# Kernel tuning notes

Measured on AMD Instinct MI355X. Metric: run time of the kernel, lower is better.

## Reference

```python
import jax, jax.numpy as jnp
import numpy as np

B, T, C, H = 4, 2048, 1024, 16
HD = C // H


def setup_inputs() -> dict:
    key = jax.random.key(0)
    ks = jax.random.split(key, 9)
    s = 1.0 / np.sqrt(C)
    return {
        "x": jax.random.normal(ks[0], (B, T, C), dtype=jnp.float32),
        "Wk": jax.random.uniform(ks[1], (C, C), jnp.float32, -s, s),
        "bk": jax.random.uniform(ks[2], (C,), jnp.float32, -s, s),
        "Wq": jax.random.uniform(ks[3], (C, C), jnp.float32, -s, s),
        "bq": jax.random.uniform(ks[4], (C,), jnp.float32, -s, s),
        "Wv": jax.random.uniform(ks[5], (C, C), jnp.float32, -s, s),
        "bv": jax.random.uniform(ks[6], (C,), jnp.float32, -s, s),
        "Wp": jax.random.uniform(ks[7], (C, C), jnp.float32, -s, s),
        "bp": jax.random.uniform(ks[8], (C,), jnp.float32, -s, s),
        "padding_mask": jnp.ones((B, T), dtype=jnp.int32),
    }


def reference(x, Wk, bk, Wq, bq, Wv, bv, Wp, bp, padding_mask):
    # torch nn.Linear: y = x @ W.T + b  (W is [out, in])
    def split_heads(t):  # [B,T,C] -> [B,H,T,HD]
        return t.reshape(B, T, H, HD).transpose(0, 2, 1, 3)

    k = split_heads(x @ Wk.T + bk)
    q = split_heads(x @ Wq.T + bq)
    v = split_heads(x @ Wv.T + bv)

    scale = 1.0 / jnp.sqrt(jnp.float32(HD))
    att = jnp.einsum("bhqd,bhkd->bhqk", q, k) * scale  # [B,H,T,T]

    causal = jnp.tril(jnp.ones((T, T), dtype=bool))  # [T,T]
    pad = (padding_mask != 0)[:, None, None, :]       # [B,1,1,T]
    mask = causal[None, None, :, :] & pad
    att = jnp.where(mask, att, -jnp.inf)
    att = jax.nn.softmax(att, axis=-1)

    y = jnp.einsum("bhqk,bhkd->bhqd", att, v)  # [B,H,T,HD]
    y = y.transpose(0, 2, 1, 3).reshape(B, T, C)
    return y @ Wp.T + bp
```

## Files before the change

kernel.cpp:

```cpp
#include <hip/hip_runtime.h>
#include <hip/hip_bf16.h>
#include <math.h>
#include <stdint.h>

#define BB 4
#define TT 2048
#define CC 1024
#define HH 16
#define HD 64
#define MM (BB*TT)
#define NQT2 16
#define SCQ 0.180336878f

using f32x2  = __attribute__((ext_vector_type(2))) float;
using f32x4  = __attribute__((ext_vector_type(4))) float;
using f32x16 = __attribute__((ext_vector_type(16))) float;
using i32x4  = __attribute__((ext_vector_type(4))) int;
using bf16x4 = __attribute__((ext_vector_type(4))) __bf16;
using bf16x8 = __attribute__((ext_vector_type(8))) __bf16;

__device__ __forceinline__ float fast_exp2(float x) {
  return __builtin_amdgcn_exp2f(x);
}

__device__ __forceinline__ int cvt_pk_bf16(float lo, float hi_) {
  int r;
  asm("v_cvt_pk_bf16_f32 %0, %1, %2" : "=v"(r) : "v"(lo), "v"(hi_));
  return r;
}

__device__ __forceinline__ f32x2 max2(f32x2 a, f32x2 b) {
  return __builtin_elementwise_max(a, b);
}

__device__ __forceinline__ void gload_lds16(const void* g, void* l) {
  __builtin_amdgcn_global_load_lds(
      (__attribute__((address_space(1))) void*)(void*)(g),
      (__attribute__((address_space(3))) void*)(l), 16, 0, 0);
}

__global__ __launch_bounds__(256)
void cvt_f32_bf16(const float* __restrict__ s, __bf16* __restrict__ d, int n4) {
  int i = blockIdx.x * 256 + threadIdx.x;
  if (i >= n4) return;
  float4 v = ((const float4*)s)[i];
  bf16x4 o;
  o[0] = (__bf16)v.x; o[1] = (__bf16)v.y; o[2] = (__bf16)v.z; o[3] = (__bf16)v.w;
  *(bf16x4*)(d + (size_t)i * 4) = o;
}

__global__ __launch_bounds__(256)
void cvt_w4(const float* __restrict__ Wq, const float* __restrict__ Wk,
            const float* __restrict__ Wv, const float* __restrict__ Wp,
            __bf16* __restrict__ wqkv, __bf16* __restrict__ wpb) {
  int which = blockIdx.y;
  const float* s = which == 0 ? Wq : which == 1 ? Wk : which == 2 ? Wv : Wp;
  __bf16* d = which == 3 ? wpb : wqkv + (size_t)which * CC * CC;
  float sc = which == 0 ? SCQ : 1.f;
  int i = blockIdx.x * 256 + threadIdx.x;
  float4 v = ((const float4*)s)[i];
  bf16x4 o;
  o[0] = (__bf16)(v.x * sc); o[1] = (__bf16)(v.y * sc);
  o[2] = (__bf16)(v.z * sc); o[3] = (__bf16)(v.w * sc);
  *(bf16x4*)(d + (size_t)i * 4) = o;
}

#define WAITV6 asm volatile("s_waitcnt vmcnt(6)" ::: "memory")
#define WAITV4 asm volatile("s_waitcnt vmcnt(4)" ::: "memory")
#define WAITV0 asm volatile("s_waitcnt vmcnt(0)" ::: "memory")
#define WAITL0 asm volatile("s_waitcnt lgkmcnt(0)" ::: "memory")
#define BARR   __builtin_amdgcn_s_barrier()
#define SB0    __builtin_amdgcn_sched_barrier(0)
#define PRIO1  __builtin_amdgcn_s_setprio(1)
#define PRIO0  __builtin_amdgcn_s_setprio(0)

#define LDA_SET(buf, mq)                                                      \
  {                                                                           \
    const char* base_ = (const char*)&LA[buf][mq][0] + (wm * 64 + lq) * 128;  \
    _Pragma("unroll")                                                         \
    for (int m4 = 0; m4 < 4; ++m4)                                            \
      _Pragma("unroll")                                                       \
      for (int kk = 0; kk < 2; ++kk)                                          \
        a[m4 * 2 + kk] =                                                      \
            *(const bf16x8*)(base_ + m4 * 2048 + ((kk * 64 + g * 16) ^ swz)); \
  }

#define LDB_SET(buf, nq)                                                      \
  {                                                                           \
    const char* base_ = (const char*)&LB[buf][nq][0] + (wn * 32 + lq) * 128;  \
    _Pragma("unroll")                                                         \
    for (int n2 = 0; n2 < 2; ++n2)                                            \
      _Pragma("unroll")                                                       \
      for (int kk = 0; kk < 2; ++kk)                                          \
        b[nq][n2 * 2 + kk] =                                                  \
            *(const bf16x8*)(base_ + n2 * 2048 + ((kk * 64 + g * 16) ^ swz)); \
  }

#define STAGE_A(nbuf, h, tt)                                                  \
  {                                                                           \
    const char* s_ = Ag + ((size_t)((h)*128 + srow)) * 2048 + (tt)*128 + scol1; \
    gload_lds16(s_, (char*)&LA[nbuf][h][0] + so16);                           \
    gload_lds16(s_ + (size_t)64 * 2048, (char*)&LA[nbuf][h][0] + so16 + 8192);\
  }

#define STAGE_B(nbuf, h, tt)                                                  \
  {                                                                           \
    const char* s_ = Bg + ((size_t)((h)*128 + srow)) * 2048 + (tt)*128 + scol1; \
    gload_lds16(s_, (char*)&LB[nbuf][h][0] + so16);                           \
    gload_lds16(s_ + (size_t)64 * 2048, (char*)&LB[nbuf][h][0] + so16 + 8192);\
  }

#define MFMA_PH(mq, nq)                                                       \
  _Pragma("unroll")                                                           \
  for (int m4 = 0; m4 < 4; ++m4)                                              \
    _Pragma("unroll")                                                         \
    for (int n2 = 0; n2 < 2; ++n2)                                            \
      _Pragma("unroll")                                                       \
      for (int kk = 0; kk < 2; ++kk)                                          \
        acc[mq][m4][nq][n2] = __builtin_amdgcn_mfma_f32_16x16x32_bf16(        \
            a[m4 * 2 + kk], b[nq][n2 * 2 + kk], acc[mq][m4][nq][n2], 0, 0, 0);

__global__ __launch_bounds__(512, 2)
void gemm_qkv(const __bf16* __restrict__ A, const __bf16* __restrict__ Bm,
              const float* __restrict__ b0, const float* __restrict__ b1,
              const float* __restrict__ b2, __bf16* __restrict__ out,
              __bf16* __restrict__ vt) {
  __shared__ __bf16 LA[2][2][128 * 64];
  __shared__ __bf16 LB[2][2][128 * 64];
  const int tid = threadIdx.x, wid = tid >> 6, lane = tid & 63;
  const int g = lane >> 4, lq = lane & 15;
  const int wm = wid >> 2, wn = wid & 3;
  const int bx0 = blockIdx.x;
  const int bx = (bx0 & 7) * 48 + (bx0 >> 3);
  const int bm = bx / 12, bn = bx % 12;
  const int brow = bm << 8, bcol = bn << 8;
  const int swz = (lq & 7) << 4;

  const int srow = tid >> 3, so16 = tid * 16;
  const int scol1 = ((tid & 7) << 4) ^ ((srow & 7) << 4);
  const char* Ag = (const char*)A + (size_t)brow * 2048;
  const char* Bg = (const char*)Bm + (size_t)bcol * 2048;

  f32x4 acc[2][4][2][2] = {};
  bf16x8 a[8], b[2][4];

  STAGE_A(0, 0, 0); STAGE_B(0, 0, 0); STAGE_B(0, 1, 0); STAGE_A(0, 1, 0);
  STAGE_A(1, 0, 1); STAGE_B(1, 0, 1); STAGE_B(1, 1, 1);
  WAITV6; BARR;

#pragma unroll 1
  for (int t = 0; t < 8; ++t) {
    const bool s2 = (t < 7);
    const int k1 = 2 * t + 1, k2 = 2 * t + 2, k3 = 2 * t + 3;
    LDA_SET(0, 0); LDB_SET(0, 0);
    STAGE_A(1, 1, k1);
    BARR; WAITL0; SB0;
    PRIO1; MFMA_PH(0, 0); PRIO0; BARR;
    LDB_SET(0, 1);
    if (s2) STAGE_A(0, 0, k2);
    BARR; WAITL0; SB0;
    PRIO1; MFMA_PH(0, 1); PRIO0; BARR;
    LDA_SET(0, 1);
    if (s2) STAGE_B(0, 0, k2);
    BARR; WAITL0; SB0;
    PRIO1; MFMA_PH(1, 1); PRIO0; BARR;
    if (s2) { STAGE_B(0, 1, k2); WAITV6; } else { WAITV0; }
    BARR; SB0;
    PRIO1; MFMA_PH(1, 0); PRIO0; BARR;
    LDA_SET(1, 0); LDB_SET(1, 0);
    if (s2) STAGE_A(0, 1, k2);
    BARR; WAITL0; SB0;
    PRIO1; MFMA_PH(0, 0); PRIO0; BARR;
    LDB_SET(1, 1);
    if (s2) STAGE_A(1, 0, k3);
    BARR; WAITL0; SB0;
    PRIO1; MFMA_PH(0, 1); PRIO0; BARR;
    LDA_SET(1, 1);
    if (s2) STAGE_B(1, 0, k3);
    BARR; WAITL0; SB0;
    PRIO1; MFMA_PH(1, 1); PRIO0; BARR;
    if (s2) { STAGE_B(1, 1, k3); WAITV6; }
    BARR; SB0;
    PRIO1; MFMA_PH(1, 0); PRIO0; BARR;
  }

  const int proj = bn >> 2;
  if (proj < 2) {
    const float* bias = proj == 0 ? b0 : b1;
    const float bsc = proj == 0 ? SCQ : 1.f;
#pragma unroll
    for (int mq = 0; mq < 2; ++mq)
#pragma unroll
      for (int nq = 0; nq < 2; ++nq)
#pragma unroll
        for (int n2 = 0; n2 < 2; ++n2) {
          int col = bcol + nq * 128 + wn * 32 + n2 * 16 + lq;
          int cw = col & (CC - 1);
          float bb = bias[cw] * bsc;
          int h_ = cw >> 6, d_ = cw & (HD - 1);
#pragma unroll
          for (int m4 = 0; m4 < 4; ++m4) {
            int row0 = brow + mq * 128 + wm * 64 + m4 * 16 + g * 4;
#pragma unroll
            for (int i = 0; i < 4; ++i) {
              int row = row0 + i;
              int b_ = row >> 11, t_ = row & (TT - 1);
              out[((size_t)proj << 23) +
                  ((((size_t)b_ * HH + h_) * TT + t_) << 6) + d_] =
                  (__bf16)(acc[mq][m4][nq][n2][i] + bb);
            }
          }
        }
  } else {
    __bf16* lt = (__bf16*)&LA[0][0][0];
    const int cv0 = (bn & 3) << 8;
    const int b_ = brow >> 11, t0 = brow & (TT - 1);
    const int hbase = (bn & 3) << 2;
    const int rd_d = tid >> 3, rd_tb = (tid & 7) << 5;
#pragma unroll
    for (int cc = 0; cc < 4; ++cc) {
      if ((wn >> 1) == (cc & 1)) {
#pragma unroll
        for (int n2 = 0; n2 < 2; ++n2) {
          int c = ((wn & 1) << 5) + (n2 << 4) + lq;
          float bb = b2[cv0 + (cc << 6) + c];
#pragma unroll
          for (int mq = 0; mq < 2; ++mq)
#pragma unroll
            for (int m4 = 0; m4 < 4; ++m4) {
              int r = (mq << 7) + (wm << 6) + (m4 << 4) + (g << 2);
              bf16x4 pk;
#pragma unroll
              for (int i = 0; i < 4; ++i)
                pk[i] = (__bf16)(acc[mq][m4][cc >> 1][n2][i] + bb);
              *(bf16x4*)(lt + c * 264 + r) = pk;
            }
        }
      }
      __syncthreads();
      __bf16* dst = vt + (((size_t)((b_ * HH + hbase + cc) * HD + rd_d)) << 11)
                       + t0 + rd_tb;
      const __bf16* srcl = lt + rd_d * 264 + rd_tb;
#pragma unroll
      for (int j = 0; j < 4; ++j)
        *(bf16x8*)(dst + j * 8) = *(const bf16x8*)(srcl + j * 8);
      __syncthreads();
    }
  }
}

__global__ __launch_bounds__(256, 2)
void gemm_proj(const __bf16* __restrict__ A, const __bf16* __restrict__ Bm,
               const float* __restrict__ bias, float* __restrict__ out,
               int M, int N, int K) {
  __shared__ __bf16 As[128 * 32];
  __shared__ __bf16 Bs[128 * 32];
  const int tid = threadIdx.x;
  const int wid = tid >> 6, lane = tid & 63;
  const int g = lane >> 4, lq = lane & 15;
  const int nbn = N >> 7;
  int bx = blockIdx.x;
  const int nb = gridDim.x;
  if ((nb & 7) == 0) { const int q = nb >> 3; bx = (bx & 7) * q + (bx >> 3); }
  const int brow = (bx / nbn) << 7;
  const int bcol = (bx % nbn) << 7;
  const int wr = (wid >> 1) << 6, wc = (wid & 1) << 6;

  f32x4 acc[4][4] = {};

  const int o0 = wid * 2048 + lane * 16;
  for (int kt = 0; kt < K; kt += 32) {
    __syncthreads();
#pragma unroll
    for (int j = 0; j < 2; ++j) {
      int o = o0 + j * 1024;
      int row = o >> 6, colb = o & 63;
      gload_lds16((const char*)A + ((size_t)(brow + row) * K + kt) * 2 + colb,
                  (char*)As + o);
      gload_lds16((const char*)Bm + ((size_t)(bcol + row) * K + kt) * 2 + colb,
                  (char*)Bs + o);
    }
    __syncthreads();
    bf16x8 av[4], bv[4];
#pragma unroll
    for (int m = 0; m < 4; ++m)
      av[m] = *(const bf16x8*)(As + (wr + m * 16 + lq) * 32 + g * 8);
#pragma unroll
    for (int n = 0; n < 4; ++n)
      bv[n] = *(const bf16x8*)(Bs + (wc + n * 16 + lq) * 32 + g * 8);
#pragma unroll
    for (int m = 0; m < 4; ++m)
#pragma unroll
      for (int n = 0; n < 4; ++n)
        acc[m][n] = __builtin_amdgcn_mfma_f32_16x16x32_bf16(av[m], bv[n], acc[m][n], 0, 0, 0);
  }

#pragma unroll
  for (int m = 0; m < 4; ++m) {
#pragma unroll
    for (int n = 0; n < 4; ++n) {
      int col = bcol + wc + n * 16 + lq;
      float bb = bias[col];
      int row0 = brow + wr + m * 16 + g * 4;
#pragma unroll
      for (int i = 0; i < 4; ++i)
        out[(size_t)(row0 + i) * N + col] = acc[m][n][i] + bb;
    }
  }
}

__global__ __launch_bounds__(256, 4)
void attn_fwd(const __bf16* __restrict__ Q, const __bf16* __restrict__ K,
              const __bf16* __restrict__ Vt, const int* __restrict__ pm,
              __bf16* __restrict__ Y) {
  __shared__ __bf16 Ks[2][64 * 64];
  __shared__ __bf16 Vs[2][64 * 64];
  __shared__ int flg;
  const int tid = threadIdx.x, wid = tid >> 6, lane = tid & 63;
  const int l31 = lane & 31, hi = lane >> 5;
  const int bx = blockIdx.x;
  const int bh = bx & 63, jj = bx >> 6;
  const int qi = 15 - (4 * (jj >> 2) + ((jj + (jj >> 2)) & 3));
  const int b_ = bh >> 4, h_ = bh & 15;
  const __bf16* Qb = Q + (size_t)bh * TT * HD;
  const __bf16* Kb = K + (size_t)bh * TT * HD;
  const __bf16* Vb = Vt + (size_t)bh * HD * TT;
  const int* pmb = pm + b_ * TT;

  const int so = tid * 16;
  const int srow = tid >> 3;
  const int scol = (so & 127) ^ ((srow & 7) << 4);

  const int q0 = qi << 7;
  const int qw = q0 + wid * 32;
  const int ntiles = 2 * qi + 2;
  const int sw0 = (l31 & 7) << 4;

  bf16x8 qf[4];
#pragma unroll
  for (int s = 0; s < 4; ++s)
    qf[s] = *(const bf16x8*)(Qb + (size_t)(qw + l31) * HD + s * 16 + hi * 8);
  SB0;

  int4 pa4 = ((const int4*)pmb)[tid];
  int4 pb4 = ((const int4*)pmb)[tid + 256];
  bool okp = pa4.x && pa4.y && pa4.z && pa4.w &&
             pb4.x && pb4.y && pb4.z && pb4.w;
  if (tid == 0) flg = 1;
  __syncthreads();
  if (!okp) flg = 0;

  {
    char* kd = (char*)&Ks[0][0] + so;
    char* vd = (char*)&Vs[0][0] + so;
#pragma unroll
    for (int j = 0; j < 2; ++j) {
      gload_lds16((const char*)Kb + (size_t)(srow + 32 * j) * 128 + scol,
                  kd + j * 4096);
      gload_lds16((const char*)Vb + (size_t)(srow + 32 * j) * (TT * 2) + scol,
                  vd + j * 4096);
    }
  }
  __syncthreads();
  const bool allones = (flg != 0);

  f32x16 o0 = {}, o1 = {};
  f32x16 vzero = {};
  float lsum = 0.f;
  float m = -INFINITY;

  int cur = 0;
#pragma unroll 1
  for (int t = 0; t < ntiles; ++t) {
    const int kv0 = t << 6;
    WAITV0;
    BARR; SB0;
    if (t + 1 < ntiles) {
      char* kd = (char*)&Ks[0][0] + (cur ^ 1) * 8192 + so;
      char* vd = (char*)&Vs[0][0] + (cur ^ 1) * 8192 + so;
      const size_t nk = (size_t)(kv0 + 64);
#pragma unroll
      for (int j = 0; j < 2; ++j) {
        gload_lds16((const char*)Kb + (nk + srow + 32 * j) * 128 + scol,
                    kd + j * 4096);
        gload_lds16((const char*)Vb + (size_t)(srow + 32 * j) * (TT * 2) +
                        nk * 2 + scol,
                    vd + j * 4096);
      }
    }

    unsigned long long bits = ~0ull;
    if (__builtin_expect(!allones, 0))
      bits = __ballot(pmb[kv0 + lane] != 0);

    if (kv0 <= qw + 31) {
      const char* VsC = (const char*)&Vs[0][0] + cur * 8192;

#pragma unroll
      for (int h = 0; h < 2; ++h) {
        const int kvh = kv0 + 32 * h;
        if (kvh <= qw + 31) {
          const char* KsC =
              (const char*)&Ks[0][0] + cur * 8192 + (32 * h + l31) * 128;
          f32x16 S;
          __builtin_amdgcn_s_setprio(1);
          {
            bf16x8 k0 = *(const bf16x8*)(KsC + ((16 * hi) ^ sw0));
            S = __builtin_amdgcn_mfma_f32_32x32x16_bf16(k0, qf[0], vzero, 0, 0, 0);
          }
#pragma unroll
          for (int s = 1; s < 4; ++s) {
            bf16x8 kf = *(const bf16x8*)(KsC + ((32 * s + 16 * hi) ^ sw0));
            S = __builtin_amdgcn_mfma_f32_32x32x16_bf16(kf, qf[s], S, 0, 0, 0);
          }
          __builtin_amdgcn_s_setprio(0);

          if (__builtin_expect(bits != ~0ull, 0)) {
#pragma unroll
            for (int r = 0; r < 16; ++r) {
              const int c = (r & 3) + 8 * (r >> 2);
              if (!((bits >> (32 * h + c + 4 * hi)) & 1ull)) S[r] = -INFINITY;
            }
          }
          if (kvh + 31 > qw) {
            const int thr = qw + l31 - kvh - 4 * hi;
#pragma unroll
            for (int r = 0; r < 16; ++r) {
              const int c = (r & 3) + 8 * (r >> 2);
              S[r] = (c <= thr) ? S[r] : -INFINITY;
            }
          }

          f32x2 x0 = {S[0], S[1]},  x1 = {S[2], S[3]};
          f32x2 x2 = {S[4], S[5]},  x3 = {S[6], S[7]};
          f32x2 x4 = {S[8], S[9]},  x5 = {S[10], S[11]};
          f32x2 x6 = {S[12], S[13]}, x7 = {S[14], S[15]};
          x0 = max2(x0, x4); x1 = max2(x1, x5);
          x2 = max2(x2, x6); x3 = max2(x3, x7);
          x0 = max2(x0, x2); x1 = max2(x1, x3);
          x0 = max2(x0, x1);
          float pmax = fmaxf(x0[0], x0[1]);
          if (!__all(pmax <= m + 8.f)) {
            float nm = fmaxf(pmax, __shfl_xor(pmax, 32));
            float mn = fmaxf(m, nm);
            float c = fast_exp2(m - mn);
            m = mn;
            lsum *= c;
#pragma unroll
            for (int r = 0; r < 16; ++r) {
              float cr = __shfl(c, (r & 3) + 8 * (r >> 2) + 4 * hi);
              o0[r] *= cr;
              o1[r] *= cr;
            }
          }

          const f32x2 mm = {m, m};
#pragma unroll
          for (int r = 0; r < 16; r += 2) {
            f32x2 u = {S[r], S[r + 1]};
            u -= mm;
            S[r] = fast_exp2(u[0]);
            S[r + 1] = fast_exp2(u[1]);
          }
          {
            f32x2 u0 = {S[0], S[1]},  u1 = {S[2], S[3]};
            f32x2 u2 = {S[4], S[5]},  u3 = {S[6], S[7]};
            f32x2 u4 = {S[8], S[9]},  u5 = {S[10], S[11]};
            f32x2 u6 = {S[12], S[13]}, u7 = {S[14], S[15]};
            u0 += u4; u1 += u5; u2 += u6; u3 += u7;
            u0 += u2; u1 += u3;
            u0 += u1;
            lsum += u0[0] + u0[1];
          }

          __builtin_amdgcn_s_setprio(1);
#pragma unroll
          for (int s = 0; s < 2; ++s) {
            int A0 = cvt_pk_bf16(S[8 * s + 0], S[8 * s + 1]);
            int A1 = cvt_pk_bf16(S[8 * s + 2], S[8 * s + 3]);
            int B0 = cvt_pk_bf16(S[8 * s + 4], S[8 * s + 5]);
            int B1 = cvt_pk_bf16(S[8 * s + 6], S[8 * s + 7]);
            int s0 = hi ? A0 : B0, s1 = hi ? A1 : B1;
            int e0 = __shfl_xor(s0, 32), e1 = __shfl_xor(s1, 32);
            i32x4 wv;
            wv[0] = hi ? e0 : A0;
            wv[1] = hi ? e1 : A1;
            wv[2] = hi ? B0 : e0;
            wv[3] = hi ? B1 : e1;
            bf16x8 pa = __builtin_bit_cast(bf16x8, wv);
            const int co = 64 * h + 32 * s + 16 * hi;
            bf16x8 v0 = *(const bf16x8*)(VsC + l31 * 128 + (co ^ sw0));
            bf16x8 v1 = *(const bf16x8*)(VsC + (32 + l31) * 128 + (co ^ sw0));
            o0 = __builtin_amdgcn_mfma_f32_32x32x16_bf16(pa, v0, o0, 0, 0, 0);
            o1 = __builtin_amdgcn_mfma_f32_32x32x16_bf16(pa, v1, o1, 0, 0, 0);
          }
          __builtin_amdgcn_s_setprio(0);
        }
      }
    }
    SB0;
    cur ^= 1;
  }

  float linv = 1.f / (lsum + __shfl_xor(lsum, 32));
#pragma unroll
  for (int r = 0; r < 16; ++r) {
    const int crow = (r & 3) + 8 * (r >> 2) + 4 * hi;
    float ir = __shfl(linv, crow);
    const int qrow = qw + crow;
    __bf16* yp = Y + ((size_t)(b_ * TT + qrow)) * CC + h_ * HD + l31;
    yp[0]  = (__bf16)(o0[r] * ir);
    yp[32] = (__bf16)(o1[r] * ir);
  }
}

extern "C" void kernel_launch(void* const* d_in, const int* in_sizes, int n_in,
                              void* d_out, int out_size, void* d_ws, size_t ws_size,
                              hipStream_t stream) {
  (void)in_sizes; (void)n_in; (void)out_size; (void)ws_size;
  const float* x  = (const float*)d_in[0];
  const float* Wk = (const float*)d_in[1];
  const float* bk = (const float*)d_in[2];
  const float* Wq = (const float*)d_in[3];
  const float* bq = (const float*)d_in[4];
  const float* Wv = (const float*)d_in[5];
  const float* bv = (const float*)d_in[6];
  const float* Wp = (const float*)d_in[7];
  const float* bp = (const float*)d_in[8];
  const int* pmask = (const int*)d_in[9];

  char* ws = (char*)d_ws;
  const size_t MB = 1024 * 1024;
  __bf16* xb   = (__bf16*)(ws);
  __bf16* wqkv = (__bf16*)(ws + 16 * MB);
  __bf16* wpb  = (__bf16*)(ws + 22 * MB);
  __bf16* qb   = (__bf16*)(ws + 24 * MB);
  __bf16* kb   = qb + ((size_t)1 << 23);
  __bf16* vtb  = (__bf16*)(ws + 56 * MB);
  __bf16* yb   = xb;

  int n4 = (MM * CC) / 4;
  cvt_f32_bf16<<<(n4 + 255) / 256, 256, 0, stream>>>(x, xb, n4);
  cvt_w4<<<dim3((CC * CC / 4) / 256, 4), 256, 0, stream>>>(
      Wq, Wk, Wv, Wp, wqkv, wpb);

  gemm_qkv<<<(MM / 256) * (3 * CC / 256), 512, 0, stream>>>(
      xb, wqkv, bq, bk, bv, qb, vtb);

  attn_fwd<<<NQT2 * BB * HH, 256, 0, stream>>>(qb, kb, vtb, pmask, yb);

  gemm_proj<<<(MM / 128) * (CC / 128), 256, 0, stream>>>(
      yb, wpb, bp, (float*)d_out, MM, CC, CC);
}
```

Before: 173.2 us.

## Shrink QKV GEMM tile from 256x256 to 256x128 and restructure pipeline

The QKV projection GEMM tile is halved in N (256x128 instead of 256x256), doubling the grid to 768 blocks. The B staging buffer, accumulator array and MFMA phases shrink to match, and the software pipeline is rescheduled with four phases per iteration instead of eight, using vmcnt(4) waits. The epilogue for Q/K and the transposed V write is adjusted for the narrower tile. This aims to cut register and LDS pressure and improve load balance across CUs, at the cost of lower arithmetic intensity and more global reads of A.

Result: no change. 173.1 us (-0.0%).

```diff
diff --git a/kernel.cpp b/kernel.cpp
--- a/kernel.cpp
+++ b/kernel.cpp
@@ -65,7 +65,6 @@
   *(bf16x4*)(d + (size_t)i * 4) = o;
 }
 
-#define WAITV6 asm volatile("s_waitcnt vmcnt(6)" ::: "memory")
 #define WAITV4 asm volatile("s_waitcnt vmcnt(4)" ::: "memory")
 #define WAITV0 asm volatile("s_waitcnt vmcnt(0)" ::: "memory")
 #define WAITL0 asm volatile("s_waitcnt lgkmcnt(0)" ::: "memory")
@@ -85,14 +84,14 @@
             *(const bf16x8*)(base_ + m4 * 2048 + ((kk * 64 + g * 16) ^ swz)); \
   }
 
-#define LDB_SET(buf, nq)                                                      \
+#define LDB_SET(buf)                                                          \
   {                                                                           \
-    const char* base_ = (const char*)&LB[buf][nq][0] + (wn * 32 + lq) * 128;  \
+    const char* base_ = (const char*)&LB[buf][0] + (wn * 32 + lq) * 128;      \
     _Pragma("unroll")                                                         \
     for (int n2 = 0; n2 < 2; ++n2)                                            \
       _Pragma("unroll")                                                       \
       for (int kk = 0; kk < 2; ++kk)                                          \
-        b[nq][n2 * 2 + kk] =                                                  \
+        b[n2 * 2 + kk] =                                                      \
             *(const bf16x8*)(base_ + n2 * 2048 + ((kk * 64 + g * 16) ^ swz)); \
   }
 
@@ -103,22 +102,22 @@
     gload_lds16(s_ + (size_t)64 * 2048, (char*)&LA[nbuf][h][0] + so16 + 8192);\
   }
 
-#define STAGE_B(nbuf, h, tt)                                                  \
+#define STAGE_B(nbuf, tt)                                                     \
   {                                                                           \
-    const char* s_ = Bg + ((size_t)((h)*128 + srow)) * 2048 + (tt)*128 + scol1; \
-    gload_lds16(s_, (char*)&LB[nbuf][h][0] + so16);                           \
-    gload_lds16(s_ + (size_t)64 * 2048, (char*)&LB[nbuf][h][0] + so16 + 8192);\
-  }
-
-#define MFMA_PH(mq, nq)                                                       \
+    const char* s_ = Bg + (size_t)srow * 2048 + (tt)*128 + scol1;             \
+    gload_lds16(s_, (char*)&LB[nbuf][0] + so16);                              \
+    gload_lds16(s_ + (size_t)64 * 2048, (char*)&LB[nbuf][0] + so16 + 8192);   \
+  }
+
+#define MFMA_PH(mq)                                                           \
   _Pragma("unroll")                                                           \
   for (int m4 = 0; m4 < 4; ++m4)                                              \
     _Pragma("unroll")                                                         \
     for (int n2 = 0; n2 < 2; ++n2)                                            \
       _Pragma("unroll")                                                       \
       for (int kk = 0; kk < 2; ++kk)                                          \
-        acc[mq][m4][nq][n2] = __builtin_amdgcn_mfma_f32_16x16x32_bf16(        \
-            a[m4 * 2 + kk], b[nq][n2 * 2 + kk], acc[mq][m4][nq][n2], 0, 0, 0);
+        acc[mq][m4][n2] = __builtin_amdgcn_mfma_f32_16x16x32_bf16(            \
+            a[m4 * 2 + kk], b[n2 * 2 + kk], acc[mq][m4][n2], 0, 0, 0);
 
 __global__ __launch_bounds__(512, 2)
 void gemm_qkv(const __bf16* __restrict__ A, const __bf16* __restrict__ Bm,
@@ -126,14 +125,14 @@
               const float* __restrict__ b2, __bf16* __restrict__ out,
               __bf16* __restrict__ vt) {
   __shared__ __bf16 LA[2][2][128 * 64];
-  __shared__ __bf16 LB[2][2][128 * 64];
+  __shared__ __bf16 LB[2][128 * 64];
   const int tid = threadIdx.x, wid = tid >> 6, lane = tid & 63;
   const int g = lane >> 4, lq = lane & 15;
   const int wm = wid >> 2, wn = wid & 3;
   const int bx0 = blockIdx.x;
-  const int bx = (bx0 & 7) * 48 + (bx0 >> 3);
-  const int bm = bx / 12, bn = bx % 12;
-  const int brow = bm << 8, bcol = bn << 8;
+  const int bx = (bx0 & 7) * 96 + (bx0 >> 3);
+  const int bm = bx / 24, bn = bx % 24;
+  const int brow = bm << 8, bcol = bn << 7;
   const int swz = (lq & 7) << 4;
 
   const int srow = tid >> 3, so16 = tid * 16;
@@ -141,85 +140,70 @@
   const char* Ag = (const char*)A + (size_t)brow * 2048;
   const char* Bg = (const char*)Bm + (size_t)bcol * 2048;
 
-  f32x4 acc[2][4][2][2] = {};
-  bf16x8 a[8], b[2][4];
-
-  STAGE_A(0, 0, 0); STAGE_B(0, 0, 0); STAGE_B(0, 1, 0); STAGE_A(0, 1, 0);
-  STAGE_A(1, 0, 1); STAGE_B(1, 0, 1); STAGE_B(1, 1, 1);
-  WAITV6; BARR;
+  f32x4 acc[2][4][2] = {};
+  bf16x8 a[8], b[4];
+
+  STAGE_A(0, 0, 0); STAGE_A(0, 1, 0); STAGE_B(0, 0);
+  STAGE_A(1, 0, 1); STAGE_B(1, 1);
+  WAITV4; BARR;
 
 #pragma unroll 1
   for (int t = 0; t < 8; ++t) {
     const bool s2 = (t < 7);
     const int k1 = 2 * t + 1, k2 = 2 * t + 2, k3 = 2 * t + 3;
-    LDA_SET(0, 0); LDB_SET(0, 0);
+    LDA_SET(0, 0); LDB_SET(0);
     STAGE_A(1, 1, k1);
     BARR; WAITL0; SB0;
-    PRIO1; MFMA_PH(0, 0); PRIO0; BARR;
-    LDB_SET(0, 1);
-    if (s2) STAGE_A(0, 0, k2);
+    PRIO1; MFMA_PH(0); PRIO0; BARR;
+    LDA_SET(0, 1);
+    if (s2) { STAGE_A(0, 0, k2); STAGE_B(0, k2); WAITV4; }
+    else    { WAITV0; }
     BARR; WAITL0; SB0;
-    PRIO1; MFMA_PH(0, 1); PRIO0; BARR;
-    LDA_SET(0, 1);
-    if (s2) STAGE_B(0, 0, k2);
-    BARR; WAITL0; SB0;
-    PRIO1; MFMA_PH(1, 1); PRIO0; BARR;
-    if (s2) { STAGE_B(0, 1, k2); WAITV6; } else { WAITV0; }
-    BARR; SB0;
-    PRIO1; MFMA_PH(1, 0); PRIO0; BARR;
-    LDA_SET(1, 0); LDB_SET(1, 0);
+    PRIO1; MFMA_PH(1); PRIO0; BARR;
+    LDA_SET(1, 0); LDB_SET(1);
     if (s2) STAGE_A(0, 1, k2);
     BARR; WAITL0; SB0;
-    PRIO1; MFMA_PH(0, 0); PRIO0; BARR;
-    LDB_SET(1, 1);
-    if (s2) STAGE_A(1, 0, k3);
+    PRIO1; MFMA_PH(0); PRIO0; BARR;
+    LDA_SET(1, 1);
+    if (s2) { STAGE_A(1, 0, k3); STAGE_B(1, k3); WAITV4; }
     BARR; WAITL0; SB0;
-    PRIO1; MFMA_PH(0, 1); PRIO0; BARR;
-    LDA_SET(1, 1);
-    if (s2) STAGE_B(1, 0, k3);
-    BARR; WAITL0; SB0;
-    PRIO1; MFMA_PH(1, 1); PRIO0; BARR;
-    if (s2) { STAGE_B(1, 1, k3); WAITV6; }
-    BARR; SB0;
-    PRIO1; MFMA_PH(1, 0); PRIO0; BARR;
-  }
-
-  const int proj = bn >> 2;
+    PRIO1; MFMA_PH(1); PRIO0; BARR;
+  }
+
+  const int proj = bn >> 3;
   if (proj < 2) {
     const float* bias = proj == 0 ? b0 : b1;
     const float bsc = proj == 0 ? SCQ : 1.f;
 #pragma unroll
     for (int mq = 0; mq < 2; ++mq)
 #pragma unroll
-      for (int nq = 0; nq < 2; ++nq)
-#pragma unroll
-        for (int n2 = 0; n2 < 2; ++n2) {
-          int col = bcol + nq * 128 + wn * 32 + n2 * 16 + lq;
-          int cw = col & (CC - 1);
-          float bb = bias[cw] * bsc;
-          int h_ = cw >> 6, d_ = cw & (HD - 1);
-#pragma unroll
-          for (int m4 = 0; m4 < 4; ++m4) {
-            int row0 = brow + mq * 128 + wm * 64 + m4 * 16 + g * 4;
-#pragma unroll
-            for (int i = 0; i < 4; ++i) {
-              int row = row0 + i;
-              int b_ = row >> 11, t_ = row & (TT - 1);
-              out[((size_t)proj << 23) +
-                  ((((size_t)b_ * HH + h_) * TT + t_) << 6) + d_] =
-                  (__bf16)(acc[mq][m4][nq][n2][i] + bb);
-            }
+      for (int n2 = 0; n2 < 2; ++n2) {
+        int col = bcol + wn * 32 + n2 * 16 + lq;
+        int cw = col & (CC - 1);
+        float bb = bias[cw] * bsc;
+        int h_ = cw >> 6, d_ = cw & (HD - 1);
+#pragma unroll
+        for (int m4 = 0; m4 < 4; ++m4) {
+          int row0 = brow + mq * 128 + wm * 64 + m4 * 16 + g * 4;
+#pragma unroll
+          for (int i = 0; i < 4; ++i) {
+            int row = row0 + i;
+            int b_ = row >> 11, t_ = row & (TT - 1);
+            out[((size_t)proj << 23) +
+                ((((size_t)b_ * HH + h_) * TT + t_) << 6) + d_] =
+                (__bf16)(acc[mq][m4][n2][i] + bb);
           }
         }
+      }
   } else {
     __bf16* lt = (__bf16*)&LA[0][0][0];
-    const int cv0 = (bn & 3) << 8;
+    const int cv0 = (bn & 7) << 7;
     const int b_ = brow >> 11, t0 = brow & (TT - 1);
-    const int hbase = (bn & 3) << 2;
+    const int hbase = (bn & 7) << 1;
     const int rd_d = tid >> 3, rd_tb = (tid & 7) << 5;
 #pragma unroll
-    for (int cc = 0; cc < 4; ++cc) {
-      if ((wn >> 1) == (cc & 1)) {
+    for (int cc = 0; cc < 2; ++cc) {
+      if ((wn >> 1) == cc) {
 #pragma unroll
         for (int n2 = 0; n2 < 2; ++n2) {
           int c = ((wn & 1) << 5) + (n2 << 4) + lq;
@@ -232,7 +216,7 @@
               bf16x4 pk;
 #pragma unroll
               for (int i = 0; i < 4; ++i)
-                pk[i] = (__bf16)(acc[mq][m4][cc >> 1][n2][i] + bb);
+                pk[i] = (__bf16)(acc[mq][m4][n2][i] + bb);
               *(bf16x4*)(lt + c * 264 + r) = pk;
             }
         }
@@ -544,7 +528,7 @@
   cvt_w4<<<dim3((CC * CC / 4) / 256, 4), 256, 0, stream>>>(
       Wq, Wk, Wv, Wp, wqkv, wpb);
 
-  gemm_qkv<<<(MM / 256) * (3 * CC / 256), 512, 0, stream>>>(
+  gemm_qkv<<<(MM / 256) * (3 * CC / 128), 512, 0, stream>>>(
       xb, wqkv, bq, bk, bv, qb, vtb);
 
   attn_fwd<<<NQT2 * BB * HH, 256, 0, stream>>>(qb, kb, vtb, pmask, yb);
```
